# Kernel optimization log

Hardware: AMD Instinct MI355X
Metric: run time of the kernel (lower is better)

## Reference

```python
import jax, jax.numpy as jnp
import numpy as np

B, G, D = 256, 14, 2048          # batch, grid, vis_embed_dim
H, A, SI, WI, ST = 1024, 512, 1024, 1024, 256  # sent_hidden, att, sent_input, word_input, int_stop
T = 10                           # max_no_of_sent


def _lin(key, out_d, in_d):
    k1, k2 = jax.random.split(key)
    return (jax.random.normal(k1, (out_d, in_d), jnp.float32) * 0.02,
            jax.random.normal(k2, (out_d,), jnp.float32) * 0.02)


def setup_inputs() -> dict:
    key = jax.random.key(0)
    ks = jax.random.split(key, 14)
    inp = {}
    inp['vis_enc_output'] = jax.random.normal(ks[0], (B, G, G, D), jnp.float32)
    inp['captions'] = jax.random.randint(ks[1], (B, T, 20), 0, 1000, jnp.int64 if jax.config.jax_enable_x64 else jnp.int32)
    inp['enc_att_w'], inp['enc_att_b'] = _lin(ks[2], A, D)
    inp['dec_att_w'], inp['dec_att_b'] = _lin(ks[3], A, H)
    inp['full_att_w'], inp['full_att_b'] = _lin(ks[4], 1, A)
    inp['ctx_w'], inp['ctx_b'] = _lin(ks[5], SI, D)
    inp['w_ih'], inp['b_ih'] = _lin(ks[6], 4 * H, SI)
    inp['w_hh'], inp['b_hh'] = _lin(ks[7], 4 * H, H)
    inp['topic_h_w'], inp['topic_h_b'] = _lin(ks[8], WI, H)
    inp['topic_c_w'], inp['topic_c_b'] = _lin(ks[9], WI, SI)
    inp['stop_p_w'], inp['stop_p_b'] = _lin(ks[10], ST, H)
    inp['stop_c_w'], inp['stop_c_b'] = _lin(ks[11], ST, H)
    inp['final_w'], inp['final_b'] = _lin(ks[12], 2, ST)
    return inp


def _forward(vis_enc_output, captions, enc_att_w, enc_att_b, dec_att_w, dec_att_b,
             full_att_w, full_att_b, ctx_w, ctx_b, w_ih, b_ih, w_hh, b_hh,
             topic_h_w, topic_h_b, topic_c_w, topic_c_b,
             stop_p_w, stop_p_b, stop_c_w, stop_c_b, final_w, final_b):
    bsz = vis_enc_output.shape[0]
    v = vis_enc_output.reshape(bsz, -1, vis_enc_output.shape[-1])  # [B, N, D]
    n_sent = captions.shape[1]
    # encoder projection is hoisted out of the loop (same math each step)
    enc_proj = jnp.einsum('bnd,ad->bna', v, enc_att_w) + enc_att_b  # [B, N, A]
    hdim = w_hh.shape[1]

    def step(carry, _):
        h, c = carry
        dec = h @ dec_att_w.T + dec_att_b                            # [B, A]
        join = jnp.tanh(enc_proj + dec[:, None, :])                  # [B, N, A]
        logits = join @ full_att_w[0] + full_att_b[0]                # [B, N]
        scores = jax.nn.softmax(logits, axis=1)
        att_out = jnp.einsum('bn,bnd->bd', scores, v)                # [B, D]
        ctx = att_out @ ctx_w.T + ctx_b                              # [B, SI]
        h_prev = h
        gates = ctx @ w_ih.T + b_ih + h @ w_hh.T + b_hh              # [B, 4H]
        i, f, g, o = jnp.split(gates, 4, axis=1)
        c_new = jax.nn.sigmoid(f) * c + jax.nn.sigmoid(i) * jnp.tanh(g)
        h_new = jax.nn.sigmoid(o) * jnp.tanh(c_new)
        topic = jnp.tanh(h_new @ topic_h_w.T + topic_h_b + ctx @ topic_c_w.T + topic_c_b)
        p = jnp.tanh(h_prev @ stop_p_w.T + stop_p_b + h_new @ stop_c_w.T + stop_c_b)
        p = p @ final_w.T + final_b                                  # [B, 2]
        return (h_new, c_new), (topic, p)

    h0 = jnp.zeros((bsz, hdim), v.dtype)
    c0 = jnp.zeros((bsz, hdim), v.dtype)
    (_, _), (topics, ps) = jax.lax.scan(step, (h0, c0), None, length=n_sent)
    return topics.transpose(1, 0, 2), ps.transpose(1, 0, 2)  # [B, T, WI], [B, T, 2]


def reference(vis_enc_output, captions, enc_att_w, enc_att_b, dec_att_w, dec_att_b,
              full_att_w, full_att_b, ctx_w, ctx_b, w_ih, b_ih, w_hh, b_hh,
              topic_h_w, topic_h_b, topic_c_w, topic_c_b,
              stop_p_w, stop_p_b, stop_c_w, stop_c_b, final_w, final_b):
    return _forward(vis_enc_output, captions, enc_att_w, enc_att_b, dec_att_w, dec_att_b,
                    full_att_w, full_att_b, ctx_w, ctx_b, w_ih, b_ih, w_hh, b_hh,
                    topic_h_w, topic_h_b, topic_c_w, topic_c_b,
                    stop_p_w, stop_p_b, stop_c_w, stop_c_b, final_w, final_b)
```

## Files before the change

kernel.cpp:

```cpp
#include <hip/hip_runtime.h>
#include <cstdint>

#define B_   256
#define NPOS 196
#define D_   2048
#define H_   1024
#define A_   512
#define T_   10

#define N13  6144
#define OFF_DEC    0
#define OFF_WHH    512
#define OFF_STOPP  4608
#define OFF_TOPICH 4864
#define OFF_STOPC  5888
#define NC   5120

#define QMAX 6.5f
#define QSINV (127.f / QMAX)
#define QS    (QMAX / 127.f)

#define PS13 ((size_t)B_ * N13)
#define PSNC ((size_t)B_ * NC)

typedef __attribute__((ext_vector_type(8))) short bf16x8;
typedef __attribute__((ext_vector_type(4))) short bf16x4;
typedef __attribute__((ext_vector_type(4))) float f32x4;

__device__ __forceinline__ float b2f(short s) {
  union { unsigned int u; float f; } c;
  c.u = ((unsigned int)(unsigned short)s) << 16;
  return c.f;
}
__device__ __forceinline__ short f2b(float f) {
  union { float f; unsigned int u; } c; c.f = f;
  unsigned int u = c.u + 0x7fffu + ((c.u >> 16) & 1u);
  return (short)(u >> 16);
}
__device__ __forceinline__ float fast_tanh(float x) {
  float a = fabsf(x);
  float e = __expf(-2.f * a);
  float t = __fdividef(1.f - e, 1.f + e);
  return x < 0.f ? -t : t;
}
__device__ __forceinline__ float fast_sigm(float x) {
  return __fdividef(1.f, 1.f + __expf(-x));
}

#define GLDS16(g, l) __builtin_amdgcn_global_load_lds( \
    (const __attribute__((address_space(1))) void*)(g), \
    (__attribute__((address_space(3))) void*)(l), 16, 0, 0)

__global__ __launch_bounds__(256) void cvtq_v_k(
    const float* __restrict__ in, short* __restrict__ v16,
    unsigned char* __restrict__ v8, long n)
{
  long i = ((long)blockIdx.x * blockDim.x + threadIdx.x) * 8;
  const long stride = (long)gridDim.x * blockDim.x * 8;
  for (; i < n; i += stride) {
    float4 a = *(const float4*)(in + i);
    float4 b = *(const float4*)(in + i + 4);
    bf16x8 o;
    o[0]=f2b(a.x); o[1]=f2b(a.y); o[2]=f2b(a.z); o[3]=f2b(a.w);
    o[4]=f2b(b.x); o[5]=f2b(b.y); o[6]=f2b(b.z); o[7]=f2b(b.w);
    *(bf16x8*)(v16 + i) = o;
    float v[8] = {a.x,a.y,a.z,a.w,b.x,b.y,b.z,b.w};
    unsigned int w0 = 0, w1 = 0;
    #pragma unroll
    for (int j = 0; j < 4; ++j) {
      float q = fminf(fmaxf(rintf(v[j] * QSINV), -127.f), 127.f) + 128.f;
      w0 |= ((unsigned int)(int)q) << (8 * j);
    }
    #pragma unroll
    for (int j = 0; j < 4; ++j) {
      float q = fminf(fmaxf(rintf(v[4+j] * QSINV), -127.f), 127.f) + 128.f;
      w1 |= ((unsigned int)(int)q) << (8 * j);
    }
    uint2 pk; pk.x = w0; pk.y = w1;
    *(uint2*)(v8 + i) = pk;
  }
}

__global__ void cvt_k(const float* __restrict__ in, short* __restrict__ out, long n)
{
  long i = ((long)blockIdx.x * blockDim.x + threadIdx.x) * 8;
  const long stride = (long)gridDim.x * blockDim.x * 8;
  for (; i < n; i += stride) {
    float4 a = *(const float4*)(in + i);
    float4 b = *(const float4*)(in + i + 4);
    bf16x8 o;
    o[0]=f2b(a.x); o[1]=f2b(a.y); o[2]=f2b(a.z); o[3]=f2b(a.w);
    o[4]=f2b(b.x); o[5]=f2b(b.y); o[6]=f2b(b.z); o[7]=f2b(b.w);
    *(bf16x8*)(out + i) = o;
  }
}

struct SegTab {
  const float* src[8];
  short* dst[8];
  int cum[9];
};
__global__ __launch_bounds__(256) void cvt_multi_k(SegTab t)
{
  int seg = 0;
  #pragma unroll
  for (int s = 0; s < 7; ++s) seg += (int)(blockIdx.x >= (unsigned)t.cum[s + 1]);
  const long i = ((long)(blockIdx.x - t.cum[seg]) * 256 + threadIdx.x) * 8;
  const float* in = t.src[seg];
  float4 a = *(const float4*)(in + i);
  float4 b = *(const float4*)(in + i + 4);
  bf16x8 o;
  o[0]=f2b(a.x); o[1]=f2b(a.y); o[2]=f2b(a.z); o[3]=f2b(a.w);
  o[4]=f2b(b.x); o[5]=f2b(b.y); o[6]=f2b(b.z); o[7]=f2b(b.w);
  *(bf16x8*)(t.dst[seg] + i) = o;
}

__global__ __launch_bounds__(256) void transpose_cvt_k(
    const float* __restrict__ in, short* __restrict__ out, int R, int C)
{
  __shared__ float t[32][33];
  const int r0 = blockIdx.y * 32, c0 = blockIdx.x * 32;
  const int tx = threadIdx.x & 31, ty = threadIdx.x >> 5;
  #pragma unroll
  for (int i = 0; i < 32; i += 8)
    t[ty + i][tx] = in[(size_t)(r0 + ty + i) * C + c0 + tx];
  __syncthreads();
  #pragma unroll
  for (int i = 0; i < 32; i += 8)
    out[(size_t)(c0 + ty + i) * R + r0 + tx] = f2b(t[tx][ty + i]);
}

__global__ __launch_bounds__(256) void biasc_k(
    const float* __restrict__ w_ih, const float* __restrict__ b_ih,
    const float* __restrict__ topic_c_w, const float* __restrict__ topic_c_b,
    const float* __restrict__ ctx_b, float* __restrict__ out)
{
  const int r = blockIdx.x * 4 + (threadIdx.x >> 6);
  const int l = threadIdx.x & 63;
  const float* wr; float bb;
  if (r < 4096) { wr = w_ih + (size_t)r * 1024;               bb = b_ih[r]; }
  else          { wr = topic_c_w + (size_t)(r - 4096) * 1024; bb = topic_c_b[r - 4096]; }
  float s = 0.f;
  #pragma unroll
  for (int k = 0; k < 16; ++k) s += wr[l + 64 * k] * ctx_b[l + 64 * k];
  #pragma unroll
  for (int o = 32; o; o >>= 1) s += __shfl_down(s, o);
  if (!l) out[r] = s + bb;
}

__global__ __launch_bounds__(256) void bias13_k(
    const float* __restrict__ dec_att_b, const float* __restrict__ b_hh,
    const float* __restrict__ stop_p_b, const float* __restrict__ topic_h_b,
    const float* __restrict__ stop_c_b, float* __restrict__ bias13)
{
  const int j = blockIdx.x * 256 + threadIdx.x;
  float v;
  if      (j < OFF_WHH)    v = dec_att_b[j];
  else if (j < OFF_STOPP)  v = b_hh[j - OFF_WHH];
  else if (j < OFF_TOPICH) v = stop_p_b[j - OFF_STOPP];
  else if (j < OFF_STOPC)  v = topic_h_b[j - OFF_TOPICH];
  else                     v = stop_c_b[j - OFF_STOPC];
  bias13[j] = v;
}

template<int OUTBF16, int BN, int SWZ, int KZ>
__global__ __launch_bounds__(256) void gemm_bt_k(
    const short* __restrict__ Aptr, const short* __restrict__ Bptr,
    const float* __restrict__ bias, void* __restrict__ Cout,
    int M, int N, int K)
{
  constexpr int TOT = 16 + BN / 8;
  constexpr int NW  = BN / 32;
  __shared__ short As[128 * 64];
  __shared__ short Bs[BN * 64];
  const int tid = threadIdx.x;
  const int l = tid & 63, wv = tid >> 6;
  const int wr = wv >> 1, wc = wv & 1;
  size_t m0, n0;
  if (SWZ) {
    const int id  = blockIdx.y * 4 + blockIdx.x;
    const int xcd = id & 7, s = id >> 3;
    m0 = (size_t)(xcd * 49 + (s >> 2)) * 128;
    n0 = (size_t)(s & 3) * BN;
  } else {
    m0 = (size_t)blockIdx.y * 128;
    n0 = (size_t)blockIdx.x * BN;
  }
  const int srow = l >> 3, scol = (l & 7) * 8;
  const int lr = l & 15, lg = l >> 4;
  const int KC = K / KZ;
  const int kbase = (KZ > 1) ? blockIdx.z * KC : 0;

  f32x4 acc[4][NW];
  #pragma unroll
  for (int i = 0; i < 4; ++i)
    #pragma unroll
    for (int j = 0; j < NW; ++j) acc[i][j] = (f32x4){0.f, 0.f, 0.f, 0.f};

  for (int k0 = kbase; k0 < kbase + KC; k0 += 64) {
    #pragma unroll
    for (int i = 0; i < TOT / 4; ++i) {
      const int c = i * 4 + wv;
      if (c < 16) {
        const int row = c * 8 + srow;
        GLDS16(Aptr + (m0 + row) * (size_t)K + k0 + scol, As + c * 512);
      } else {
        const int row = (c - 16) * 8 + srow;
        GLDS16(Bptr + (n0 + row) * (size_t)K + k0 + scol, Bs + (c - 16) * 512);
      }
    }
    __syncthreads();
    #pragma unroll
    for (int kk = 0; kk < 64; kk += 32) {
      bf16x8 af[4], bfr[NW];
      #pragma unroll
      for (int m = 0; m < 4; ++m)
        af[m] = *(const bf16x8*)(As + (wr * 64 + m * 16 + lr) * 64 + kk + lg * 8);
      #pragma unroll
      for (int n = 0; n < NW; ++n)
        bfr[n] = *(const bf16x8*)(Bs + (wc * (BN / 2) + n * 16 + lr) * 64 + kk + lg * 8);
      #pragma unroll
      for (int m = 0; m < 4; ++m)
        #pragma unroll
        for (int n = 0; n < NW; ++n)
          acc[m][n] = __builtin_amdgcn_mfma_f32_16x16x32_bf16(af[m], bfr[n], acc[m][n], 0, 0, 0);
    }
    __syncthreads();
  }

  #pragma unroll
  for (int m = 0; m < 4; ++m) {
    const size_t row = m0 + wr * 64 + m * 16 + lg * 4;
    #pragma unroll
    for (int n = 0; n < NW; ++n) {
      const size_t col = n0 + wc * (BN / 2) + n * 16 + lr;
      if (KZ > 1) {
        float* Cp = (float*)Cout + (size_t)blockIdx.z * M * (size_t)N;
        #pragma unroll
        for (int r = 0; r < 4; ++r)
          Cp[(row + r) * (size_t)N + col] = acc[m][n][r];
      } else {
        const float bv = bias[col];
        #pragma unroll
        for (int r = 0; r < 4; ++r) {
          const float v = acc[m][n][r] + bv;
          if (OUTBF16) ((short*)Cout)[(row + r) * (size_t)N + col] = f2b(v);
          else         ((float*)Cout)[(row + r) * (size_t)N + col] = v;
        }
      }
    }
  }
}

template<int DO_FINAL, int DO_SCORES>
__global__ __launch_bounds__(512) void sf_k(
    const float* __restrict__ pcur, const float* __restrict__ pprev,
    const float* __restrict__ g3p, const float* __restrict__ biasc,
    const float* __restrict__ bias13,
    const short* __restrict__ encp, const float* __restrict__ fullw,
    const float* __restrict__ finw, const float* __restrict__ finb,
    float* __restrict__ scbuf, float* __restrict__ out_t,
    float* __restrict__ out_p, int tprev)
{
  const int b = blockIdx.x, tid = threadIdx.x;
  const int l = tid & 63, wv = tid >> 6;
  const size_t b13 = (size_t)b * N13;
  __shared__ float dec_s[A_], fw_s[A_], sc[NPOS], red[16], pp[256];

  if (DO_FINAL) {
    float* ot = out_t + (size_t)b * (T_ * 1024) + (size_t)tprev * 1024;
    #pragma unroll
    for (int i = 0; i < 2; ++i) {
      const int j = tid + i * 512;
      float th = bias13[OFF_TOPICH + j] + pcur[b13 + OFF_TOPICH + j]
               + pcur[PS13 + b13 + OFF_TOPICH + j];
      float tc = biasc[4096 + j];
      #pragma unroll
      for (int z = 0; z < 4; ++z) tc += g3p[z * PSNC + (size_t)b * NC + 4096 + j];
      ot[j] = fast_tanh(th + tc);
    }
    if (tid < 256) {
      float a = bias13[OFF_STOPP + tid] + pprev[b13 + OFF_STOPP + tid]
              + pprev[PS13 + b13 + OFF_STOPP + tid];
      float c = bias13[OFF_STOPC + tid] + pcur[b13 + OFF_STOPC + tid]
              + pcur[PS13 + b13 + OFF_STOPC + tid];
      pp[tid] = fast_tanh(a + c);
    }
  }
  if (DO_SCORES && tid < A_) {
    dec_s[tid] = pcur[b13 + tid] + pcur[PS13 + b13 + tid] + bias13[tid];
    fw_s[tid]  = fullw[tid];
  }
  __syncthreads();

  if (DO_FINAL && wv < 2) {
    float s = 0.f;
    #pragma unroll
    for (int k = 0; k < 4; ++k) s += pp[l + 64 * k] * finw[wv * 256 + l + 64 * k];
    #pragma unroll
    for (int o = 32; o; o >>= 1) s += __shfl_down(s, o);
    if (!l) out_p[(size_t)b * (T_ * 2) + tprev * 2 + wv] = s + finb[wv];
  }

  if (DO_SCORES) {
    const short* ep = encp + (size_t)b * NPOS * A_;
    for (int n = wv; n < NPOS; n += 8) {
      bf16x8 e = *(const bf16x8*)(ep + (size_t)n * A_ + l * 8);
      float s = 0.f;
      #pragma unroll
      for (int j = 0; j < 8; ++j)
        s += fast_tanh(b2f(e[j]) + dec_s[l * 8 + j]) * fw_s[l * 8 + j];
      #pragma unroll
      for (int o = 32; o; o >>= 1) s += __shfl_down(s, o);
      if (!l) sc[n] = s;
    }
    __syncthreads();

    float lm = (tid < NPOS) ? sc[tid] : -3e38f;
    #pragma unroll
    for (int o = 32; o; o >>= 1) lm = fmaxf(lm, __shfl_down(lm, o));
    if (!l) red[wv] = lm;
    __syncthreads();
    float mx = red[0];
    #pragma unroll
    for (int i = 1; i < 8; ++i) mx = fmaxf(mx, red[i]);
    const float ev = (tid < NPOS) ? __expf(sc[tid] - mx) : 0.f;
    float es = ev;
    #pragma unroll
    for (int o = 32; o; o >>= 1) es += __shfl_down(es, o);
    if (!l) red[8 + wv] = es;
    __syncthreads();
    float tot = red[8];
    #pragma unroll
    for (int i = 1; i < 8; ++i) tot += red[8 + i];
    if (tid < NPOS) scbuf[(size_t)b * NPOS + tid] = ev * __fdividef(1.f, tot);
  }
}

template<int VMODE>
__global__ __launch_bounds__(256) void pv_k(
    const void* __restrict__ vptr, const float* __restrict__ scbuf,
    short* __restrict__ attout)
{
  const int b = blockIdx.y;
  const int dbase = blockIdx.x * 1024;
  const int tid = threadIdx.x;
  const int grp = tid >> 7;
  const int dt = (tid & 127) * 8;
  __shared__ float sc[NPOS];
  __shared__ float tmp[1024];
  if (tid < NPOS) sc[tid] = scbuf[(size_t)b * NPOS + tid];
  __syncthreads();

  float a[8] = {0,0,0,0,0,0,0,0};
  if (VMODE == 1) {
    const unsigned char* vb = (const unsigned char*)vptr
        + (size_t)b * NPOS * D_ + dbase + dt;
    #pragma unroll 8
    for (int n = grp; n < NPOS; n += 2) {
      const float s = sc[n];
      const uint2 w = *(const uint2*)(vb + (size_t)n * D_);
      a[0] += s * (float)(w.x & 255u);
      a[1] += s * (float)((w.x >> 8) & 255u);
      a[2] += s * (float)((w.x >> 16) & 255u);
      a[3] += s * (float)(w.x >> 24);
      a[4] += s * (float)(w.y & 255u);
      a[5] += s * (float)((w.y >> 8) & 255u);
      a[6] += s * (float)((w.y >> 16) & 255u);
      a[7] += s * (float)(w.y >> 24);
    }
  } else {
    const float* vf = (const float*)vptr + (size_t)b * NPOS * D_ + dbase + dt;
    #pragma unroll 2
    for (int n = grp; n < NPOS; n += 2) {
      const float s = sc[n];
      float4 v0 = *(const float4*)(vf + (size_t)n * D_);
      float4 v1 = *(const float4*)(vf + (size_t)n * D_ + 4);
      a[0] += s*v0.x; a[1] += s*v0.y; a[2] += s*v0.z; a[3] += s*v0.w;
      a[4] += s*v1.x; a[5] += s*v1.y; a[6] += s*v1.z; a[7] += s*v1.w;
    }
  }
  if (grp == 1) {
    #pragma unroll
    for (int j = 0; j < 8; ++j) tmp[dt + j] = a[j];
  }
  __syncthreads();
  if (grp == 0) {
    bf16x8 o8;
    #pragma unroll
    for (int j = 0; j < 8; ++j) {
      float v = a[j] + tmp[dt + j];
      if (VMODE == 1) v = v * QS - 128.f * QS;
      o8[j] = f2b(v);
    }
    *(bf16x8*)(attout + (size_t)b * D_ + dbase + dt) = o8;
  }
}

__global__ __launch_bounds__(256) void lstm_k(
    const float* __restrict__ g3p, const float* __restrict__ gPp,
    const float* __restrict__ biasc, const float* __restrict__ bias13,
    float* __restrict__ c, short* __restrict__ hbf)
{
  const int idx = (blockIdx.x * 256 + threadIdx.x) * 4;
  const int b = idx >> 10, j = idx & 1023;
  f32x4 gate[4];
  #pragma unroll
  for (int g = 0; g < 4; ++g) {
    const size_t base  = (size_t)b * NC + g * 1024 + j;
    const size_t baseh = (size_t)b * N13 + OFF_WHH + g * 1024 + j;
    f32x4 s = *(const f32x4*)(biasc + g * 1024 + j);
    s += *(const f32x4*)(bias13 + OFF_WHH + g * 1024 + j);
    #pragma unroll
    for (int z = 0; z < 4; ++z) s += *(const f32x4*)(g3p + z * PSNC + base);
    #pragma unroll
    for (int z = 0; z < 2; ++z) s += *(const f32x4*)(gPp + z * PS13 + baseh);
    gate[g] = s;
  }
  f32x4 cv = *(const f32x4*)(c + idx);
  f32x4 cn;
  bf16x4 hn;
  #pragma unroll
  for (int k = 0; k < 4; ++k) {
    const float nc2 = fast_sigm(gate[1][k]) * cv[k]
                    + fast_sigm(gate[0][k]) * fast_tanh(gate[2][k]);
    cn[k] = nc2;
    hn[k] = f2b(fast_sigm(gate[3][k]) * fast_tanh(nc2));
  }
  *(f32x4*)(c + idx) = cn;
  *(bf16x4*)(hbf + idx) = hn;
}

extern "C" void kernel_launch(void* const* d_in, const int* in_sizes, int n_in,
                              void* d_out, int out_size, void* d_ws, size_t ws_size,
                              hipStream_t stream)
{
  const float* vis       = (const float*)d_in[0];
  const float* enc_att_w = (const float*)d_in[2];
  const float* enc_att_b = (const float*)d_in[3];
  const float* dec_att_w = (const float*)d_in[4];
  const float* dec_att_b = (const float*)d_in[5];
  const float* full_att_w= (const float*)d_in[6];
  const float* ctx_w     = (const float*)d_in[8];
  const float* ctx_b     = (const float*)d_in[9];
  const float* w_ih      = (const float*)d_in[10];
  const float* b_ih      = (const float*)d_in[11];
  const float* w_hh      = (const float*)d_in[12];
  const float* b_hh      = (const float*)d_in[13];
  const float* topic_h_w = (const float*)d_in[14];
  const float* topic_h_b = (const float*)d_in[15];
  const float* topic_c_w = (const float*)d_in[16];
  const float* topic_c_b = (const float*)d_in[17];
  const float* stop_p_w  = (const float*)d_in[18];
  const float* stop_p_b  = (const float*)d_in[19];
  const float* stop_c_w  = (const float*)d_in[20];
  const float* stop_c_b  = (const float*)d_in[21];
  const float* final_w   = (const float*)d_in[22];
  const float* final_b   = (const float*)d_in[23];

  uint8_t* wsp = (uint8_t*)d_ws;
  size_t off = 0;
  auto take = [&](size_t bytes) -> void* {
    void* p = wsp + off;
    off = (off + bytes + 255) & ~(size_t)255;
    return p;
  };

  short* encproj = (short*)take((size_t)B_ * NPOS * A_ * 2);
  short* encw    = (short*)take((size_t)A_ * D_ * 2);
  short* w2cat   = (short*)take((size_t)NC * 1024 * 2);
  short* ctxwT   = (short*)take((size_t)D_ * 1024 * 2);
  short* Wc      = (short*)take((size_t)NC * D_ * 2);
  short* w13     = (short*)take((size_t)N13 * H_ * 2);
  float* biasc   = (float*)take((size_t)NC * 4);
  float* bias13  = (float*)take((size_t)N13 * 4);
  float* zeros   = (float*)take((size_t)D_ * 4);
  short* hbf     = (short*)take((size_t)B_ * H_ * 2);
  float* cst     = (float*)take((size_t)B_ * H_ * 4);
  float* pairs0  = (float*)take(2 * PS13 * 4);
  float* pairs1  = (float*)take(2 * PS13 * 4);
  float* g3p     = (float*)take(4 * PSNC * 4);
  short* attb    = (short*)take((size_t)B_ * D_ * 2);
  float* scbuf   = (float*)take((size_t)B_ * NPOS * 4);
  const size_t base0 = off;
  const long   nv = (long)B_ * NPOS * D_;
  unsigned char* v8 = (unsigned char*)take((size_t)nv);
  short* v16 = (short*)(wsp + off);
  const bool full = (ws_size >= off + (size_t)nv * 2);

  float* out_t = (float*)d_out;
  float* out_p = (float*)d_out + (size_t)B_ * T_ * 1024;

  {
    SegTab t;
    const float* srcs[8] = {enc_att_w, w_ih, topic_c_w, dec_att_w, w_hh,
                            stop_p_w, topic_h_w, stop_c_w};
    short* dsts[8] = {encw, w2cat, w2cat + (size_t)4096 * 1024,
                      w13 + (size_t)OFF_DEC * 1024, w13 + (size_t)OFF_WHH * 1024,
                      w13 + (size_t)OFF_STOPP * 1024, w13 + (size_t)OFF_TOPICH * 1024,
                      w13 + (size_t)OFF_STOPC * 1024};
    const int nel[8] = {1048576, 4194304, 1048576, 524288, 4194304, 262144, 1048576, 262144};
    int c = 0;
    for (int i = 0; i < 8; ++i) {
      t.src[i] = srcs[i]; t.dst[i] = dsts[i];
      t.cum[i] = c; c += nel[i] / 2048;
    }
    t.cum[8] = c;
    cvt_multi_k<<<c, 256, 0, stream>>>(t);
  }
  transpose_cvt_k<<<dim3(D_ / 32, 1024 / 32), 256, 0, stream>>>(ctx_w, ctxwT, 1024, D_);
  hipMemsetAsync(zeros, 0, (size_t)D_ * 4, stream);
  gemm_bt_k<1, 128, 0, 1><<<dim3(D_ / 128, NC / 128), 256, 0, stream>>>(
      w2cat, ctxwT, zeros, Wc, NC, D_, 1024);
  biasc_k<<<NC / 4, 256, 0, stream>>>(w_ih, b_ih, topic_c_w, topic_c_b, ctx_b, biasc);
  bias13_k<<<N13 / 256, 256, 0, stream>>>(
      dec_att_b, b_hh, stop_p_b, topic_h_b, stop_c_b, bias13);
  hipMemsetAsync(cst, 0, (size_t)B_ * H_ * 4, stream);
  hipMemsetAsync(pairs1, 0, 2 * PS13 * 4, stream);

  const int Mrows = B_ * NPOS;
  if (full) {
    cvtq_v_k<<<8192, 256, 0, stream>>>(vis, v16, v8, nv);
    gemm_bt_k<1, 128, 1, 1><<<dim3(A_ / 128, Mrows / 128), 256, 0, stream>>>(
        v16, encw, enc_att_b, encproj, Mrows, A_, D_);
  } else {
    const size_t avail = (ws_size > base0) ? ws_size - base0 : 0;
    int dt = 1;
    const int cand[] = {56, 28, 14, 8, 7, 4, 2, 1};
    for (int c : cand)
      if ((392 % c) == 0 && (size_t)c * 128 * D_ * 2 <= avail) { dt = c; break; }
    short* vchunk = (short*)(wsp + base0);
    const int CR = dt * 128;
    for (int s = 0; s < Mrows; s += CR) {
      cvt_k<<<4096, 256, 0, stream>>>(vis + (size_t)s * D_, vchunk, (long)CR * D_);
      gemm_bt_k<1, 128, 0, 1><<<dim3(A_ / 128, dt), 256, 0, stream>>>(
          vchunk, encw, enc_att_b, encproj + (size_t)s * A_, CR, A_, D_);
    }
  }

  for (int t = 0; t < T_; ++t) {
    float* pcur  = (t & 1) ? pairs0 : pairs1;
    float* pprev = (t & 1) ? pairs1 : pairs0;
    if (t == 0)
      sf_k<0, 1><<<B_, 512, 0, stream>>>(pcur, pprev, g3p, biasc, bias13,
          encproj, full_att_w, final_w, final_b, scbuf, out_t, out_p, 0);
    else
      sf_k<1, 1><<<B_, 512, 0, stream>>>(pcur, pprev, g3p, biasc, bias13,
          encproj, full_att_w, final_w, final_b, scbuf, out_t, out_p, t - 1);
    if (full) pv_k<1><<<dim3(2, B_), 256, 0, stream>>>(v8, scbuf, attb);
    else      pv_k<0><<<dim3(2, B_), 256, 0, stream>>>(vis, scbuf, attb);
    gemm_bt_k<0, 32, 0, 4><<<dim3(NC / 32, B_ / 128, 4), 256, 0, stream>>>(
        attb, Wc, nullptr, g3p, B_, NC, D_);
    lstm_k<<<(B_ * H_) / 1024, 256, 0, stream>>>(g3p, pcur, biasc, bias13, cst, hbf);
    float* pnew = (t & 1) ? pairs1 : pairs0;
    gemm_bt_k<0, 32, 0, 2><<<dim3(N13 / 32, B_ / 128, 2), 256, 0, stream>>>(
        hbf, w13, nullptr, pnew, B_, N13, H_);
  }
  {
    float* pcur  = ((T_ - 1) & 1) ? pairs1 : pairs0;
    float* pprev = ((T_ - 1) & 1) ? pairs0 : pairs1;
    sf_k<1, 0><<<B_, 512, 0, stream>>>(pcur, pprev, g3p, biasc, bias13,
        encproj, full_att_w, final_w, final_b, scbuf, out_t, out_p, T_ - 1);
  }
}
```

Measured before the change: 1.170 ms.

## Fuse softmax with attention pooling, double-buffer step GEMMs, retile LSTM launch

Merges the softmax-score kernel and the weighted pooling kernel into one per-batch kernel, so scores stay in shared memory and the scbuf round trip and one launch per step go away. Adds a double-buffered LDS path to the GEMM, used by the per-step GEMMs, which now run with BN=64 tiles instead of 32. Also halves the LSTM block size. In exchange, the fused kernel pools over 196 positions serially with only 256 blocks, and the wider tiles produce fewer GEMM blocks, both of which may reduce parallelism.

```diff
diff --git a/kernel.cpp b/kernel.cpp
--- a/kernel.cpp
+++ b/kernel.cpp
@@ -163,7 +163,7 @@
   bias13[j] = v;
 }
 
-template<int OUTBF16, int BN, int SWZ, int KZ>
+template<int OUTBF16, int BN, int SWZ, int KZ, int DBUF>
 __global__ __launch_bounds__(256) void gemm_bt_k(
     const short* __restrict__ Aptr, const short* __restrict__ Bptr,
     const float* __restrict__ bias, void* __restrict__ Cout,
@@ -171,8 +171,9 @@
 {
   constexpr int TOT = 16 + BN / 8;
   constexpr int NW  = BN / 32;
-  __shared__ short As[128 * 64];
-  __shared__ short Bs[BN * 64];
+  constexpr int NB  = DBUF ? 2 : 1;
+  __shared__ short As[NB * 128 * 64];
+  __shared__ short Bs[NB * BN * 64];
   const int tid = threadIdx.x;
   const int l = tid & 63, wv = tid >> 6;
   const int wr = wv >> 1, wc = wv & 1;
@@ -190,6 +191,7 @@
   const int lr = l & 15, lg = l >> 4;
   const int KC = K / KZ;
   const int kbase = (KZ > 1) ? blockIdx.z * KC : 0;
+  const int kend  = kbase + KC;
 
   f32x4 acc[4][NW];
   #pragma unroll
@@ -197,35 +199,58 @@
     #pragma unroll
     for (int j = 0; j < NW; ++j) acc[i][j] = (f32x4){0.f, 0.f, 0.f, 0.f};
 
-  for (int k0 = kbase; k0 < kbase + KC; k0 += 64) {
+  auto stage = [&](int buf, int k0) {
+    short* Ab = As + buf * (128 * 64);
+    short* Bb = Bs + buf * (BN * 64);
     #pragma unroll
     for (int i = 0; i < TOT / 4; ++i) {
       const int c = i * 4 + wv;
       if (c < 16) {
         const int row = c * 8 + srow;
-        GLDS16(Aptr + (m0 + row) * (size_t)K + k0 + scol, As + c * 512);
+        GLDS16(Aptr + (m0 + row) * (size_t)K + k0 + scol, Ab + c * 512);
       } else {
         const int row = (c - 16) * 8 + srow;
-        GLDS16(Bptr + (n0 + row) * (size_t)K + k0 + scol, Bs + (c - 16) * 512);
+        GLDS16(Bptr + (n0 + row) * (size_t)K + k0 + scol, Bb + (c - 16) * 512);
       }
     }
-    __syncthreads();
+  };
+  auto compute = [&](int buf) {
+    const short* Ab = As + buf * (128 * 64);
+    const short* Bb = Bs + buf * (BN * 64);
     #pragma unroll
     for (int kk = 0; kk < 64; kk += 32) {
       bf16x8 af[4], bfr[NW];
       #pragma unroll
       for (int m = 0; m < 4; ++m)
-        af[m] = *(const bf16x8*)(As + (wr * 64 + m * 16 + lr) * 64 + kk + lg * 8);
+        af[m] = *(const bf16x8*)(Ab + (wr * 64 + m * 16 + lr) * 64 + kk + lg * 8);
       #pragma unroll
       for (int n = 0; n < NW; ++n)
-        bfr[n] = *(const bf16x8*)(Bs + (wc * (BN / 2) + n * 16 + lr) * 64 + kk + lg * 8);
+        bfr[n] = *(const bf16x8*)(Bb + (wc * (BN / 2) + n * 16 + lr) * 64 + kk + lg * 8);
       #pragma unroll
       for (int m = 0; m < 4; ++m)
         #pragma unroll
         for (int n = 0; n < NW; ++n)
           acc[m][n] = __builtin_amdgcn_mfma_f32_16x16x32_bf16(af[m], bfr[n], acc[m][n], 0, 0, 0);
     }
+  };
+
+  if (DBUF) {
+    stage(0, kbase);
     __syncthreads();
+    int cur = 0;
+    for (int k0 = kbase; k0 < kend; k0 += 64) {
+      if (k0 + 64 < kend) stage(cur ^ 1, k0 + 64);
+      compute(cur);
+      __syncthreads();
+      cur ^= 1;
+    }
+  } else {
+    for (int k0 = kbase; k0 < kend; k0 += 64) {
+      stage(0, k0);
+      __syncthreads();
+      compute(0);
+      __syncthreads();
+    }
   }
 
   #pragma unroll
@@ -252,15 +277,15 @@
   }
 }
 
-template<int DO_FINAL, int DO_SCORES>
-__global__ __launch_bounds__(512) void sf_k(
+template<int DO_FINAL, int DO_SCORES, int VMODE>
+__global__ __launch_bounds__(512) void sfpv_k(
     const float* __restrict__ pcur, const float* __restrict__ pprev,
     const float* __restrict__ g3p, const float* __restrict__ biasc,
     const float* __restrict__ bias13,
     const short* __restrict__ encp, const float* __restrict__ fullw,
     const float* __restrict__ finw, const float* __restrict__ finb,
-    float* __restrict__ scbuf, float* __restrict__ out_t,
-    float* __restrict__ out_p, int tprev)
+    const void* __restrict__ vptr, short* __restrict__ attout,
+    float* __restrict__ out_t, float* __restrict__ out_p, int tprev)
 {
   const int b = blockIdx.x, tid = threadIdx.x;
   const int l = tid & 63, wv = tid >> 6;
@@ -333,76 +358,50 @@
     float tot = red[8];
     #pragma unroll
     for (int i = 1; i < 8; ++i) tot += red[8 + i];
-    if (tid < NPOS) scbuf[(size_t)b * NPOS + tid] = ev * __fdividef(1.f, tot);
-  }
-}
-
-template<int VMODE>
-__global__ __launch_bounds__(256) void pv_k(
-    const void* __restrict__ vptr, const float* __restrict__ scbuf,
-    short* __restrict__ attout)
-{
-  const int b = blockIdx.y;
-  const int dbase = blockIdx.x * 1024;
-  const int tid = threadIdx.x;
-  const int grp = tid >> 7;
-  const int dt = (tid & 127) * 8;
-  __shared__ float sc[NPOS];
-  __shared__ float tmp[1024];
-  if (tid < NPOS) sc[tid] = scbuf[(size_t)b * NPOS + tid];
-  __syncthreads();
-
-  float a[8] = {0,0,0,0,0,0,0,0};
-  if (VMODE == 1) {
-    const unsigned char* vb = (const unsigned char*)vptr
-        + (size_t)b * NPOS * D_ + dbase + dt;
-    #pragma unroll 8
-    for (int n = grp; n < NPOS; n += 2) {
-      const float s = sc[n];
-      const uint2 w = *(const uint2*)(vb + (size_t)n * D_);
-      a[0] += s * (float)(w.x & 255u);
-      a[1] += s * (float)((w.x >> 8) & 255u);
-      a[2] += s * (float)((w.x >> 16) & 255u);
-      a[3] += s * (float)(w.x >> 24);
-      a[4] += s * (float)(w.y & 255u);
-      a[5] += s * (float)((w.y >> 8) & 255u);
-      a[6] += s * (float)((w.y >> 16) & 255u);
-      a[7] += s * (float)(w.y >> 24);
-    }
-  } else {
-    const float* vf = (const float*)vptr + (size_t)b * NPOS * D_ + dbase + dt;
-    #pragma unroll 2
-    for (int n = grp; n < NPOS; n += 2) {
-      const float s = sc[n];
-      float4 v0 = *(const float4*)(vf + (size_t)n * D_);
-      float4 v1 = *(const float4*)(vf + (size_t)n * D_ + 4);
-      a[0] += s*v0.x; a[1] += s*v0.y; a[2] += s*v0.z; a[3] += s*v0.w;
-      a[4] += s*v1.x; a[5] += s*v1.y; a[6] += s*v1.z; a[7] += s*v1.w;
-    }
-  }
-  if (grp == 1) {
-    #pragma unroll
-    for (int j = 0; j < 8; ++j) tmp[dt + j] = a[j];
-  }
-  __syncthreads();
-  if (grp == 0) {
-    bf16x8 o8;
-    #pragma unroll
-    for (int j = 0; j < 8; ++j) {
-      float v = a[j] + tmp[dt + j];
-      if (VMODE == 1) v = v * QS - 128.f * QS;
-      o8[j] = f2b(v);
-    }
-    *(bf16x8*)(attout + (size_t)b * D_ + dbase + dt) = o8;
-  }
-}
-
-__global__ __launch_bounds__(256) void lstm_k(
+    if (tid < NPOS) sc[tid] = ev * __fdividef(1.f, tot);
+    __syncthreads();
+
+    const int d0 = tid * 4;
+    float a0 = 0.f, a1 = 0.f, a2 = 0.f, a3 = 0.f;
+    if (VMODE == 1) {
+      const unsigned char* vb = (const unsigned char*)vptr
+          + (size_t)b * NPOS * D_ + d0;
+      #pragma unroll 4
+      for (int n = 0; n < NPOS; ++n) {
+        const float s = sc[n];
+        const unsigned int w = *(const unsigned int*)(vb + (size_t)n * D_);
+        a0 += s * (float)(w & 255u);
+        a1 += s * (float)((w >> 8) & 255u);
+        a2 += s * (float)((w >> 16) & 255u);
+        a3 += s * (float)(w >> 24);
+      }
+    } else {
+      const float* vf = (const float*)vptr + (size_t)b * NPOS * D_ + d0;
+      #pragma unroll 2
+      for (int n = 0; n < NPOS; ++n) {
+        const float s = sc[n];
+        float4 vv = *(const float4*)(vf + (size_t)n * D_);
+        a0 += s * vv.x; a1 += s * vv.y; a2 += s * vv.z; a3 += s * vv.w;
+      }
+    }
+    bf16x4 o4;
+    if (VMODE == 1) {
+      const float offs = -128.f * QS;
+      o4[0] = f2b(a0 * QS + offs); o4[1] = f2b(a1 * QS + offs);
+      o4[2] = f2b(a2 * QS + offs); o4[3] = f2b(a3 * QS + offs);
+    } else {
+      o4[0] = f2b(a0); o4[1] = f2b(a1); o4[2] = f2b(a2); o4[3] = f2b(a3);
+    }
+    *(bf16x4*)(attout + (size_t)b * D_ + d0) = o4;
+  }
+}
+
+__global__ __launch_bounds__(128) void lstm_k(
     const float* __restrict__ g3p, const float* __restrict__ gPp,
     const float* __restrict__ biasc, const float* __restrict__ bias13,
     float* __restrict__ c, short* __restrict__ hbf)
 {
-  const int idx = (blockIdx.x * 256 + threadIdx.x) * 4;
+  const int idx = (blockIdx.x * 128 + threadIdx.x) * 4;
   const int b = idx >> 10, j = idx & 1023;
   f32x4 gate[4];
   #pragma unroll
@@ -481,7 +480,6 @@
   float* pairs1  = (float*)take(2 * PS13 * 4);
   float* g3p     = (float*)take(4 * PSNC * 4);
   short* attb    = (short*)take((size_t)B_ * D_ * 2);
-  float* scbuf   = (float*)take((size_t)B_ * NPOS * 4);
   const size_t base0 = off;
   const long   nv = (long)B_ * NPOS * D_;
   unsigned char* v8 = (unsigned char*)take((size_t)nv);
@@ -510,7 +508,7 @@
   }
   transpose_cvt_k<<<dim3(D_ / 32, 1024 / 32), 256, 0, stream>>>(ctx_w, ctxwT, 1024, D_);
   hipMemsetAsync(zeros, 0, (size_t)D_ * 4, stream);
-  gemm_bt_k<1, 128, 0, 1><<<dim3(D_ / 128, NC / 128), 256, 0, stream>>>(
+  gemm_bt_k<1, 128, 0, 1, 0><<<dim3(D_ / 128, NC / 128), 256, 0, stream>>>(
       w2cat, ctxwT, zeros, Wc, NC, D_, 1024);
   biasc_k<<<NC / 4, 256, 0, stream>>>(w_ih, b_ih, topic_c_w, topic_c_b, ctx_b, biasc);
   bias13_k<<<N13 / 256, 256, 0, stream>>>(
@@ -521,7 +519,7 @@
   const int Mrows = B_ * NPOS;
   if (full) {
     cvtq_v_k<<<8192, 256, 0, stream>>>(vis, v16, v8, nv);
-    gemm_bt_k<1, 128, 1, 1><<<dim3(A_ / 128, Mrows / 128), 256, 0, stream>>>(
+    gemm_bt_k<1, 128, 1, 1, 0><<<dim3(A_ / 128, Mrows / 128), 256, 0, stream>>>(
         v16, encw, enc_att_b, encproj, Mrows, A_, D_);
   } else {
     const size_t avail = (ws_size > base0) ? ws_size - base0 : 0;
@@ -533,7 +531,7 @@
     const int CR = dt * 128;
     for (int s = 0; s < Mrows; s += CR) {
       cvt_k<<<4096, 256, 0, stream>>>(vis + (size_t)s * D_, vchunk, (long)CR * D_);
-      gemm_bt_k<1, 128, 0, 1><<<dim3(A_ / 128, dt), 256, 0, stream>>>(
+      gemm_bt_k<1, 128, 0, 1, 0><<<dim3(A_ / 128, dt), 256, 0, stream>>>(
           vchunk, encw, enc_att_b, encproj + (size_t)s * A_, CR, A_, D_);
     }
   }
@@ -541,25 +539,33 @@
   for (int t = 0; t < T_; ++t) {
     float* pcur  = (t & 1) ? pairs0 : pairs1;
     float* pprev = (t & 1) ? pairs1 : pairs0;
-    if (t == 0)
-      sf_k<0, 1><<<B_, 512, 0, stream>>>(pcur, pprev, g3p, biasc, bias13,
-          encproj, full_att_w, final_w, final_b, scbuf, out_t, out_p, 0);
-    else
-      sf_k<1, 1><<<B_, 512, 0, stream>>>(pcur, pprev, g3p, biasc, bias13,
-          encproj, full_att_w, final_w, final_b, scbuf, out_t, out_p, t - 1);
-    if (full) pv_k<1><<<dim3(2, B_), 256, 0, stream>>>(v8, scbuf, attb);
-    else      pv_k<0><<<dim3(2, B_), 256, 0, stream>>>(vis, scbuf, attb);
-    gemm_bt_k<0, 32, 0, 4><<<dim3(NC / 32, B_ / 128, 4), 256, 0, stream>>>(
+    const void* vp = full ? (const void*)v8 : (const void*)vis;
+    if (t == 0) {
+      if (full)
+        sfpv_k<0, 1, 1><<<B_, 512, 0, stream>>>(pcur, pprev, g3p, biasc, bias13,
+            encproj, full_att_w, final_w, final_b, vp, attb, out_t, out_p, 0);
+      else
+        sfpv_k<0, 1, 0><<<B_, 512, 0, stream>>>(pcur, pprev, g3p, biasc, bias13,
+            encproj, full_att_w, final_w, final_b, vp, attb, out_t, out_p, 0);
+    } else {
+      if (full)
+        sfpv_k<1, 1, 1><<<B_, 512, 0, stream>>>(pcur, pprev, g3p, biasc, bias13,
+            encproj, full_att_w, final_w, final_b, vp, attb, out_t, out_p, t - 1);
+      else
+        sfpv_k<1, 1, 0><<<B_, 512, 0, stream>>>(pcur, pprev, g3p, biasc, bias13,
+            encproj, full_att_w, final_w, final_b, vp, attb, out_t, out_p, t - 1);
+    }
+    gemm_bt_k<0, 64, 0, 4, 1><<<dim3(NC / 64, B_ / 128, 4), 256, 0, stream>>>(
         attb, Wc, nullptr, g3p, B_, NC, D_);
-    lstm_k<<<(B_ * H_) / 1024, 256, 0, stream>>>(g3p, pcur, biasc, bias13, cst, hbf);
+    lstm_k<<<(B_ * H_) / 512, 128, 0, stream>>>(g3p, pcur, biasc, bias13, cst, hbf);
     float* pnew = (t & 1) ? pairs1 : pairs0;
-    gemm_bt_k<0, 32, 0, 2><<<dim3(N13 / 32, B_ / 128, 2), 256, 0, stream>>>(
+    gemm_bt_k<0, 64, 0, 2, 1><<<dim3(N13 / 64, B_ / 128, 2), 256, 0, stream>>>(
         hbf, w13, nullptr, pnew, B_, N13, H_);
   }
   {
     float* pcur  = ((T_ - 1) & 1) ? pairs1 : pairs0;
     float* pprev = ((T_ - 1) & 1) ? pairs0 : pairs1;
-    sf_k<1, 0><<<B_, 512, 0, stream>>>(pcur, pprev, g3p, biasc, bias13,
-        encproj, full_att_w, final_w, final_b, scbuf, out_t, out_p, T_ - 1);
-  }
-}
+    sfpv_k<1, 0, 0><<<B_, 512, 0, stream>>>(pcur, pprev, g3p, biasc, bias13,
+        encproj, full_att_w, final_w, final_b, nullptr, attb, out_t, out_p, T_ - 1);
+  }
+}
```

Measured after the change: 1.197 ms. 2.3% more time.
